# Optimization experiments

Hardware: AMD Instinct MI355X
Metric: run time of the kernel (lower is better)

## Reference

```python
import jax, jax.numpy as jnp
import numpy as np

B = 1_000_000  # batch size
A = 40         # number of CelebA face attributes
GAMMA = 2.0
EPS = 1e-12


def setup_inputs() -> dict:
    key = jax.random.key(0)
    k1, k2, k3 = jax.random.split(key, 3)
    inputs = jax.random.uniform(k1, (B, A), dtype=jnp.float32)  # probabilities
    targets = jax.random.randint(k2, (A, B), 0, 2, dtype=jnp.int32)  # binary labels, attr-first layout
    attr_loss_weight = jax.random.uniform(k3, (A,), dtype=jnp.float32) + 0.5  # positive per-attr weights
    return {"inputs": inputs, "targets": targets, "attr_loss_weight": attr_loss_weight}


def reference(inputs, targets, attr_loss_weight):
    # inputs: [B, A] probabilities; targets: [A, B] binary labels
    t = targets.T.astype(inputs.dtype)                      # [B, A]
    p = jnp.clip(inputs, EPS, 1.0 - EPS)
    bce = -(t * jnp.log(p) + (1.0 - t) * jnp.log1p(-p))     # elementwise BCE
    w = attr_loss_weight[None, :] * jnp.power(1.0 - inputs, GAMMA)  # focal weight
    # per-sample mean over attributes (F.binary_cross_entropy default), summed over batch
    loss = jnp.sum(jnp.mean(w * bce, axis=1))
    return loss
```

## Files before the change

kernel.cpp:

```cpp
#include <hip/hip_runtime.h>

#define NB 1000000
#define NA 40
#define TILE 256
#define NTILES ((NB + TILE - 1) / TILE)
#define NEG_LN2_OVER_A (-0.017328679513998632f)

__global__ __launch_bounds__(256, 4) void focal_loss_kernel(
    const float* __restrict__ inputs,
    const int*   __restrict__ targets,
    const float* __restrict__ attr_w,
    float* __restrict__ out)
{
    __shared__ unsigned int s_t[NA * 65];
    __shared__ float s_aw[NA];
    __shared__ float s_red[TILE / 64];

    const int t  = threadIdx.x;
    const int b0 = blockIdx.x * TILE;

    if (t < NA) s_aw[t] = attr_w[t] * NEG_LN2_OVER_A;

    float acc = 0.0f;

    if (blockIdx.x != NTILES - 1) {
        int4 v[10];
        #pragma unroll
        for (int j = 0; j < 10; ++j) {
            const int q  = t + TILE * j;
            const int a  = q >> 6;
            const int t4 = q & 63;
            v[j] = *(const int4*)(targets + (size_t)a * NB + (b0 + 4 * t4));
        }
        const float4* in4 = (const float4*)inputs + (size_t)b0 * 10;
        float4 xv[10];
        #pragma unroll
        for (int j = 0; j < 10; ++j) xv[j] = in4[t + TILE * j];

        #pragma unroll
        for (int j = 0; j < 10; ++j) {
            const int q  = t + TILE * j;
            const int a  = q >> 6;
            const int t4 = q & 63;
            s_t[a * 65 + t4] =  (unsigned)(v[j].x & 1)        | ((unsigned)(v[j].y & 1) << 8)
                             | ((unsigned)(v[j].z & 1) << 16) | ((unsigned)(v[j].w & 1) << 24);
        }
        __syncthreads();

        const unsigned char* st8 = (const unsigned char*)s_t;
        #pragma unroll
        for (int j = 0; j < 10; ++j) {
            const int f = t + TILE * j;
            const int s = f / 10;
            const int r = 4 * (f - s * 10);
            const float xs[4] = {xv[j].x, xv[j].y, xv[j].z, xv[j].w};
            #pragma unroll
            for (int k = 0; k < 4; ++k) {
                const float x   = xs[k];
                const float om  = 1.0f - x;
                const float w   = s_aw[r + k] * (om * om);
                const float p   = fmaxf(x,  1e-12f);
                const float q0  = fmaxf(om, 1e-12f);
                const float sel = st8[(r + k) * 260 + s] ? p : q0;
                acc = fmaf(w, __log2f(sel), acc);
            }
        }
    } else {
        #pragma unroll
        for (int j = 0; j < 10; ++j) {
            const int q  = t + TILE * j;
            const int a  = q >> 6;
            const int t4 = q & 63;
            const int base = b0 + 4 * t4;
            unsigned int pack = 0;
            for (int k = 0; k < 4; ++k)
                if (base + k < NB)
                    pack |= (unsigned)(targets[(size_t)a * NB + base + k] & 1) << (8 * k);
            s_t[a * 65 + t4] = pack;
        }
        __syncthreads();
        const unsigned char* st8 = (const unsigned char*)s_t;
        const float4* in4 = (const float4*)inputs + (size_t)b0 * 10;
        #pragma unroll
        for (int j = 0; j < 10; ++j) {
            const int f = t + TILE * j;
            const int s = f / 10;
            const int r = 4 * (f - s * 10);
            if (b0 + s < NB) {
                const float4 x4 = in4[f];
                const float xs[4] = {x4.x, x4.y, x4.z, x4.w};
                #pragma unroll
                for (int k = 0; k < 4; ++k) {
                    const float x   = xs[k];
                    const float om  = 1.0f - x;
                    const float w   = s_aw[r + k] * (om * om);
                    const float p   = fmaxf(x,  1e-12f);
                    const float q0  = fmaxf(om, 1e-12f);
                    const float sel = st8[(r + k) * 260 + s] ? p : q0;
                    acc = fmaf(w, __log2f(sel), acc);
                }
            }
        }
    }

    float vsum = acc;
    #pragma unroll
    for (int off = 32; off > 0; off >>= 1)
        vsum += __shfl_xor(vsum, off, 64);
    if ((t & 63) == 0) s_red[t >> 6] = vsum;
    __syncthreads();
    if (t == 0) {
        float r2 = 0.0f;
        #pragma unroll
        for (int w2 = 0; w2 < TILE / 64; ++w2) r2 += s_red[w2];
        atomicAdd(out, r2);
    }
}

extern "C" void kernel_launch(void* const* d_in, const int* in_sizes, int n_in,
                              void* d_out, int out_size, void* d_ws, size_t ws_size,
                              hipStream_t stream) {
    const float* inputs  = (const float*)d_in[0];
    const int*   targets = (const int*)d_in[1];
    const float* attr_w  = (const float*)d_in[2];
    float* out = (float*)d_out;
    hipMemsetAsync(out, 0, sizeof(float), stream);
    focal_loss_kernel<<<dim3(NTILES), dim3(TILE), 0, stream>>>(inputs, targets, attr_w, out);
}
```

Before: 325.2 us.

## Process four tiles per block with double-buffered target prefetch

Each block now handles four consecutive 256-sample tiles, prefetching the next tile's targets into registers during compute and staging the packed bits in a double-buffered LDS array. This aims to hide global load latency and amortize block setup and the final atomic. The grid shrinks roughly fourfold, which reduces the number of resident waves available to hide latency and adds a serial dependency within each block.

```diff
diff --git a/kernel.cpp b/kernel.cpp
--- a/kernel.cpp
+++ b/kernel.cpp
@@ -3,7 +3,9 @@
 #define NB 1000000
 #define NA 40
 #define TILE 256
-#define NTILES ((NB + TILE - 1) / TILE)
+#define G 4
+#define SPB (TILE * G)
+#define NBLK ((NB + SPB - 1) / SPB)
 #define NEG_LN2_OVER_A (-0.017328679513998632f)
 
 __global__ __launch_bounds__(256, 4) void focal_loss_kernel(
@@ -12,83 +14,57 @@
     const float* __restrict__ attr_w,
     float* __restrict__ out)
 {
-    __shared__ unsigned int s_t[NA * 65];
+    __shared__ unsigned int s_t[2][NA * 65];
     __shared__ float s_aw[NA];
     __shared__ float s_red[TILE / 64];
 
     const int t  = threadIdx.x;
-    const int b0 = blockIdx.x * TILE;
+    const int B0 = blockIdx.x * SPB;
 
     if (t < NA) s_aw[t] = attr_w[t] * NEG_LN2_OVER_A;
 
     float acc = 0.0f;
 
-    if (blockIdx.x != NTILES - 1) {
-        int4 v[10];
-        #pragma unroll
-        for (int j = 0; j < 10; ++j) {
-            const int q  = t + TILE * j;
-            const int a  = q >> 6;
-            const int t4 = q & 63;
-            v[j] = *(const int4*)(targets + (size_t)a * NB + (b0 + 4 * t4));
-        }
-        const float4* in4 = (const float4*)inputs + (size_t)b0 * 10;
+    if (blockIdx.x != NBLK - 1) {
+        int4   v[10];
         float4 xv[10];
-        #pragma unroll
-        for (int j = 0; j < 10; ++j) xv[j] = in4[t + TILE * j];
+        const float4* in4 = (const float4*)inputs;
 
         #pragma unroll
         for (int j = 0; j < 10; ++j) {
-            const int q  = t + TILE * j;
-            const int a  = q >> 6;
-            const int t4 = q & 63;
-            s_t[a * 65 + t4] =  (unsigned)(v[j].x & 1)        | ((unsigned)(v[j].y & 1) << 8)
-                             | ((unsigned)(v[j].z & 1) << 16) | ((unsigned)(v[j].w & 1) << 24);
+            const int q = t + TILE * j, a = q >> 6, t4 = q & 63;
+            v[j] = *(const int4*)(targets + (size_t)a * NB + (B0 + 4 * t4));
+        }
+        #pragma unroll
+        for (int j = 0; j < 10; ++j)
+            xv[j] = in4[(size_t)B0 * 10 + t + TILE * j];
+        #pragma unroll
+        for (int j = 0; j < 10; ++j) {
+            const int q = t + TILE * j, a = q >> 6, t4 = q & 63;
+            s_t[0][a * 65 + t4] = (unsigned)(v[j].x & 1)        | ((unsigned)(v[j].y & 1) << 8)
+                                | ((unsigned)(v[j].z & 1) << 16) | ((unsigned)(v[j].w & 1) << 24);
         }
         __syncthreads();
 
-        const unsigned char* st8 = (const unsigned char*)s_t;
         #pragma unroll
-        for (int j = 0; j < 10; ++j) {
-            const int f = t + TILE * j;
-            const int s = f / 10;
-            const int r = 4 * (f - s * 10);
-            const float xs[4] = {xv[j].x, xv[j].y, xv[j].z, xv[j].w};
+        for (int g = 0; g < G; ++g) {
+            const int bt_next = B0 + TILE * (g + 1);
+
+            if (g < G - 1) {
+                #pragma unroll
+                for (int j = 0; j < 10; ++j) {
+                    const int q = t + TILE * j, a = q >> 6, t4 = q & 63;
+                    v[j] = *(const int4*)(targets + (size_t)a * NB + (bt_next + 4 * t4));
+                }
+            }
+
+            const unsigned char* st8 = (const unsigned char*)s_t[g & 1];
             #pragma unroll
-            for (int k = 0; k < 4; ++k) {
-                const float x   = xs[k];
-                const float om  = 1.0f - x;
-                const float w   = s_aw[r + k] * (om * om);
-                const float p   = fmaxf(x,  1e-12f);
-                const float q0  = fmaxf(om, 1e-12f);
-                const float sel = st8[(r + k) * 260 + s] ? p : q0;
-                acc = fmaf(w, __log2f(sel), acc);
-            }
-        }
-    } else {
-        #pragma unroll
-        for (int j = 0; j < 10; ++j) {
-            const int q  = t + TILE * j;
-            const int a  = q >> 6;
-            const int t4 = q & 63;
-            const int base = b0 + 4 * t4;
-            unsigned int pack = 0;
-            for (int k = 0; k < 4; ++k)
-                if (base + k < NB)
-                    pack |= (unsigned)(targets[(size_t)a * NB + base + k] & 1) << (8 * k);
-            s_t[a * 65 + t4] = pack;
-        }
-        __syncthreads();
-        const unsigned char* st8 = (const unsigned char*)s_t;
-        const float4* in4 = (const float4*)inputs + (size_t)b0 * 10;
-        #pragma unroll
-        for (int j = 0; j < 10; ++j) {
-            const int f = t + TILE * j;
-            const int s = f / 10;
-            const int r = 4 * (f - s * 10);
-            if (b0 + s < NB) {
-                const float4 x4 = in4[f];
-                const float xs[4] = {x4.x, x4.y, x4.z, x4.w};
+            for (int j = 0; j < 10; ++j) {
+                const int f = t + TILE * j;
+                const int s = f / 10;
+                const int r = 4 * (f - s * 10);
+                const float xs[4] = {xv[j].x, xv[j].y, xv[j].z, xv[j].w};
                 #pragma unroll
                 for (int k = 0; k < 4; ++k) {
                     const float x   = xs[k];
@@ -98,6 +74,59 @@
                     const float q0  = fmaxf(om, 1e-12f);
                     const float sel = st8[(r + k) * 260 + s] ? p : q0;
                     acc = fmaf(w, __log2f(sel), acc);
+                }
+            }
+
+            if (g < G - 1) {
+                #pragma unroll
+                for (int j = 0; j < 10; ++j)
+                    xv[j] = in4[(size_t)bt_next * 10 + t + TILE * j];
+                #pragma unroll
+                for (int j = 0; j < 10; ++j) {
+                    const int q = t + TILE * j, a = q >> 6, t4 = q & 63;
+                    s_t[(g + 1) & 1][a * 65 + t4] =
+                          (unsigned)(v[j].x & 1)        | ((unsigned)(v[j].y & 1) << 8)
+                        | ((unsigned)(v[j].z & 1) << 16) | ((unsigned)(v[j].w & 1) << 24);
+                }
+                __syncthreads();
+            }
+        }
+    } else {
+        for (int g = 0; g < G; ++g) {
+            const int bt = B0 + TILE * g;
+            if (bt >= NB) break;
+            __syncthreads();
+            #pragma unroll
+            for (int j = 0; j < 10; ++j) {
+                const int q = t + TILE * j, a = q >> 6, t4 = q & 63;
+                const int base = bt + 4 * t4;
+                unsigned int pack = 0;
+                for (int k = 0; k < 4; ++k)
+                    if (base + k < NB)
+                        pack |= (unsigned)(targets[(size_t)a * NB + base + k] & 1) << (8 * k);
+                s_t[0][a * 65 + t4] = pack;
+            }
+            __syncthreads();
+            const unsigned char* st8 = (const unsigned char*)s_t[0];
+            const float4* in4t = (const float4*)inputs + (size_t)bt * 10;
+            #pragma unroll
+            for (int j = 0; j < 10; ++j) {
+                const int f = t + TILE * j;
+                const int s = f / 10;
+                const int r = 4 * (f - s * 10);
+                if (bt + s < NB) {
+                    const float4 x4 = in4t[f];
+                    const float xs[4] = {x4.x, x4.y, x4.z, x4.w};
+                    #pragma unroll
+                    for (int k = 0; k < 4; ++k) {
+                        const float x   = xs[k];
+                        const float om  = 1.0f - x;
+                        const float w   = s_aw[r + k] * (om * om);
+                        const float p   = fmaxf(x,  1e-12f);
+                        const float q0  = fmaxf(om, 1e-12f);
+                        const float sel = st8[(r + k) * 260 + s] ? p : q0;
+                        acc = fmaf(w, __log2f(sel), acc);
+                    }
                 }
             }
         }
@@ -125,5 +154,5 @@
     const float* attr_w  = (const float*)d_in[2];
     float* out = (float*)d_out;
     hipMemsetAsync(out, 0, sizeof(float), stream);
-    focal_loss_kernel<<<dim3(NTILES), dim3(TILE), 0, stream>>>(inputs, targets, attr_w, out);
+    focal_loss_kernel<<<dim3(NBLK), dim3(TILE), 0, stream>>>(inputs, targets, attr_w, out);
 }
```

Result: slower. 350.3 us (+7.7%).

## Persistent blocks with double-buffered async global-to-LDS target loads

Applied to the files above, without the earlier changes.

Replaces the one-tile-per-block grid with 768 persistent 128-thread blocks, each looping over a contiguous range of 128-sample tiles. Target tiles are copied straight into a double-buffered LDS array with global_load_lds, and the next tile is prefetched while the current one is computed. Each thread now owns one sample row (10 float4 loads) and reads its 40 targets directly from LDS, so the byte-packing step goes away. The aim is to hide global-memory latency and cut launch and packing overhead. In exchange, far fewer waves are resident, the per-thread input loads are strided and less coalesced, and correctness depends on the async LDS copies finishing before the barrier.

```diff
diff --git a/kernel.cpp b/kernel.cpp
--- a/kernel.cpp
+++ b/kernel.cpp
@@ -2,103 +2,123 @@
 
 #define NB 1000000
 #define NA 40
-#define TILE 256
-#define NTILES ((NB + TILE - 1) / TILE)
+#define BTH 128
+#define NT_FULL (NB / BTH)
+#define TAIL_START (NT_FULL * BTH)
+#define TAIL_N (NB - TAIL_START)
+#define NBLK 768
+#define QT (NT_FULL / NBLK)
+#define RT (NT_FULL % NBLK)
 #define NEG_LN2_OVER_A (-0.017328679513998632f)
 
-__global__ __launch_bounds__(256, 4) void focal_loss_kernel(
+
+typedef __attribute__((address_space(1))) const void gas_t;
+typedef __attribute__((address_space(3))) void las_t;
+
+__device__ __forceinline__ void gll16(const void* g, void* l) {
+    __builtin_amdgcn_global_load_lds((gas_t*)g, (las_t*)l, 16, 0, 0);
+}
+
+__global__ __launch_bounds__(BTH, 2) void focal_loss_kernel(
     const float* __restrict__ inputs,
     const int*   __restrict__ targets,
     const float* __restrict__ attr_w,
     float* __restrict__ out)
 {
-    __shared__ unsigned int s_t[NA * 65];
+    __shared__ unsigned int s_t[2][NA * BTH];
     __shared__ float s_aw[NA];
-    __shared__ float s_red[TILE / 64];
+    __shared__ float s_red[BTH / 64];
 
-    const int t  = threadIdx.x;
-    const int b0 = blockIdx.x * TILE;
+    const int t = threadIdx.x;
+    const int w = t >> 6;
+    const int l = t & 63;
 
     if (t < NA) s_aw[t] = attr_w[t] * NEG_LN2_OVER_A;
 
+    const int b  = blockIdx.x;
+    const int t0 = b * QT + (b < RT ? b : RT);
+    const int nt = QT + (b < RT ? 1 : 0);
+
     float acc = 0.0f;
+    const float4* in4 = (const float4*)inputs;
 
-    if (blockIdx.x != NTILES - 1) {
-        int4 v[10];
+    float4 xv[10];
+
+    {
+        const int b0 = t0 * BTH;
+        #pragma unroll
+        for (int r = 0; r < 10; ++r) {
+            const int i = w * 10 + r;
+            const int a = 2 * i + (l >> 5);
+            const int s = b0 + 4 * (l & 31);
+            gll16(targets + (size_t)a * NB + s,
+                  (char*)&s_t[0][0] + (size_t)i * 1024);
+        }
+        #pragma unroll
+        for (int j = 0; j < 10; ++j)
+            xv[j] = in4[(size_t)(b0 + t) * 10 + j];
+    }
+    __syncthreads();
+
+    int buf = 0;
+    for (int it = 0; it < nt; ++it) {
+        if (it + 1 < nt) {
+            const int b0n = (t0 + it + 1) * BTH;
+            #pragma unroll
+            for (int r = 0; r < 10; ++r) {
+                const int i = w * 10 + r;
+                const int a = 2 * i + (l >> 5);
+                const int s = b0n + 4 * (l & 31);
+                gll16(targets + (size_t)a * NB + s,
+                      (char*)&s_t[buf ^ 1][0] + (size_t)i * 1024);
+            }
+        }
+
+        const unsigned int* st = &s_t[buf][0];
         #pragma unroll
         for (int j = 0; j < 10; ++j) {
-            const int q  = t + TILE * j;
-            const int a  = q >> 6;
-            const int t4 = q & 63;
-            v[j] = *(const int4*)(targets + (size_t)a * NB + (b0 + 4 * t4));
-        }
-        const float4* in4 = (const float4*)inputs + (size_t)b0 * 10;
-        float4 xv[10];
-        #pragma unroll
-        for (int j = 0; j < 10; ++j) xv[j] = in4[t + TILE * j];
-
-        #pragma unroll
-        for (int j = 0; j < 10; ++j) {
-            const int q  = t + TILE * j;
-            const int a  = q >> 6;
-            const int t4 = q & 63;
-            s_t[a * 65 + t4] =  (unsigned)(v[j].x & 1)        | ((unsigned)(v[j].y & 1) << 8)
-                             | ((unsigned)(v[j].z & 1) << 16) | ((unsigned)(v[j].w & 1) << 24);
-        }
-        __syncthreads();
-
-        const unsigned char* st8 = (const unsigned char*)s_t;
-        #pragma unroll
-        for (int j = 0; j < 10; ++j) {
-            const int f = t + TILE * j;
-            const int s = f / 10;
-            const int r = 4 * (f - s * 10);
             const float xs[4] = {xv[j].x, xv[j].y, xv[j].z, xv[j].w};
             #pragma unroll
             for (int k = 0; k < 4; ++k) {
+                const int a   = 4 * j + k;
                 const float x   = xs[k];
                 const float om  = 1.0f - x;
-                const float w   = s_aw[r + k] * (om * om);
+                const float wgt = s_aw[a] * (om * om);
                 const float p   = fmaxf(x,  1e-12f);
                 const float q0  = fmaxf(om, 1e-12f);
-                const float sel = st8[(r + k) * 260 + s] ? p : q0;
-                acc = fmaf(w, __log2f(sel), acc);
+                const float sel = st[a * BTH + t] ? p : q0;
+                acc = fmaf(wgt, __log2f(sel), acc);
             }
         }
-    } else {
+
+        if (it + 1 < nt) {
+            const int b0n = (t0 + it + 1) * BTH;
+            #pragma unroll
+            for (int j = 0; j < 10; ++j)
+                xv[j] = in4[(size_t)(b0n + t) * 10 + j];
+        }
+        __syncthreads();
+        buf ^= 1;
+    }
+
+    if (b == NBLK - 1 && t < TAIL_N) {
+        const int s = TAIL_START + t;
+        float4 tx[10];
+        #pragma unroll
+        for (int j = 0; j < 10; ++j) tx[j] = in4[(size_t)s * 10 + j];
         #pragma unroll
         for (int j = 0; j < 10; ++j) {
-            const int q  = t + TILE * j;
-            const int a  = q >> 6;
-            const int t4 = q & 63;
-            const int base = b0 + 4 * t4;
-            unsigned int pack = 0;
-            for (int k = 0; k < 4; ++k)
-                if (base + k < NB)
-                    pack |= (unsigned)(targets[(size_t)a * NB + base + k] & 1) << (8 * k);
-            s_t[a * 65 + t4] = pack;
-        }
-        __syncthreads();
-        const unsigned char* st8 = (const unsigned char*)s_t;
-        const float4* in4 = (const float4*)inputs + (size_t)b0 * 10;
-        #pragma unroll
-        for (int j = 0; j < 10; ++j) {
-            const int f = t + TILE * j;
-            const int s = f / 10;
-            const int r = 4 * (f - s * 10);
-            if (b0 + s < NB) {
-                const float4 x4 = in4[f];
-                const float xs[4] = {x4.x, x4.y, x4.z, x4.w};
-                #pragma unroll
-                for (int k = 0; k < 4; ++k) {
-                    const float x   = xs[k];
-                    const float om  = 1.0f - x;
-                    const float w   = s_aw[r + k] * (om * om);
-                    const float p   = fmaxf(x,  1e-12f);
-                    const float q0  = fmaxf(om, 1e-12f);
-                    const float sel = st8[(r + k) * 260 + s] ? p : q0;
-                    acc = fmaf(w, __log2f(sel), acc);
-                }
+            const float xs[4] = {tx[j].x, tx[j].y, tx[j].z, tx[j].w};
+            #pragma unroll
+            for (int k = 0; k < 4; ++k) {
+                const int a   = 4 * j + k;
+                const float x   = xs[k];
+                const float om  = 1.0f - x;
+                const float wgt = s_aw[a] * (om * om);
+                const float p   = fmaxf(x,  1e-12f);
+                const float q0  = fmaxf(om, 1e-12f);
+                const float sel = targets[(size_t)a * NB + s] ? p : q0;
+                acc = fmaf(wgt, __log2f(sel), acc);
             }
         }
     }
@@ -107,14 +127,9 @@
     #pragma unroll
     for (int off = 32; off > 0; off >>= 1)
         vsum += __shfl_xor(vsum, off, 64);
-    if ((t & 63) == 0) s_red[t >> 6] = vsum;
+    if (l == 0) s_red[w] = vsum;
     __syncthreads();
-    if (t == 0) {
-        float r2 = 0.0f;
-        #pragma unroll
-        for (int w2 = 0; w2 < TILE / 64; ++w2) r2 += s_red[w2];
-        atomicAdd(out, r2);
-    }
+    if (t == 0) atomicAdd(out, s_red[0] + s_red[1]);
 }
 
 extern "C" void kernel_launch(void* const* d_in, const int* in_sizes, int n_in,
@@ -125,5 +140,5 @@
     const float* attr_w  = (const float*)d_in[2];
     float* out = (float*)d_out;
     hipMemsetAsync(out, 0, sizeof(float), stream);
-    focal_loss_kernel<<<dim3(NTILES), dim3(TILE), 0, stream>>>(inputs, targets, attr_w, out);
+    focal_loss_kernel<<<dim3(NBLK), dim3(BTH), 0, stream>>>(inputs, targets, attr_w, out);
 }
```

Result: no change. 330.4 us (+1.6%).

## Map one sample per thread and drop shared-memory target transpose

Applied to the files above, without the earlier changes.

Replaces the tiled shared-memory transpose of packed targets with a one-thread-per-sample scheme. Each thread reads its own 40 input probabilities as float4s and reads targets straight from global memory with coalesced column accesses. Loads are software-pipelined three groups ahead of the compute, and occupancy is raised to 8 blocks per CU. This removes the LDS writes, byte reads and barrier, but each thread's input loads are now strided by 160 bytes, so a wave touches many cache lines per load instruction.

```diff
diff --git a/kernel.cpp b/kernel.cpp
--- a/kernel.cpp
+++ b/kernel.cpp
@@ -2,106 +2,59 @@
 
 #define NB 1000000
 #define NA 40
-#define TILE 256
-#define NTILES ((NB + TILE - 1) / TILE)
+#define BTH 256
+#define NBLK ((NB + BTH - 1) / BTH)
 #define NEG_LN2_OVER_A (-0.017328679513998632f)
 
-__global__ __launch_bounds__(256, 4) void focal_loss_kernel(
+__global__ __launch_bounds__(BTH, 8) void focal_loss_kernel(
     const float* __restrict__ inputs,
     const int*   __restrict__ targets,
     const float* __restrict__ attr_w,
     float* __restrict__ out)
 {
-    __shared__ unsigned int s_t[NA * 65];
     __shared__ float s_aw[NA];
-    __shared__ float s_red[TILE / 64];
+    __shared__ float s_red[BTH / 64];
 
-    const int t  = threadIdx.x;
-    const int b0 = blockIdx.x * TILE;
+    const int t = threadIdx.x;
+    if (t < NA) s_aw[t] = attr_w[t] * NEG_LN2_OVER_A;
+    __syncthreads();
 
-    if (t < NA) s_aw[t] = attr_w[t] * NEG_LN2_OVER_A;
+    const int s  = blockIdx.x * BTH + t;
+    const int ok = (s < NB);
+    const int sc = ok ? s : (NB - 1);
 
-    float acc = 0.0f;
+    const float4* xr = (const float4*)(inputs + (size_t)sc * NA);
 
-    if (blockIdx.x != NTILES - 1) {
-        int4 v[10];
-        #pragma unroll
-        for (int j = 0; j < 10; ++j) {
-            const int q  = t + TILE * j;
-            const int a  = q >> 6;
-            const int t4 = q & 63;
-            v[j] = *(const int4*)(targets + (size_t)a * NB + (b0 + 4 * t4));
+    float4 xq[4];
+    int    tq[4][4];
+    float  acc = 0.0f;
+
+    #pragma unroll
+    for (int g = 0; g < 13; ++g) {
+        if (g < 10) {
+            const int sl = g & 3;
+            xq[sl] = xr[g];
+            #pragma unroll
+            for (int k = 0; k < 4; ++k)
+                tq[sl][k] = targets[(size_t)(4 * g + k) * NB + sc];
         }
-        const float4* in4 = (const float4*)inputs + (size_t)b0 * 10;
-        float4 xv[10];
-        #pragma unroll
-        for (int j = 0; j < 10; ++j) xv[j] = in4[t + TILE * j];
-
-        #pragma unroll
-        for (int j = 0; j < 10; ++j) {
-            const int q  = t + TILE * j;
-            const int a  = q >> 6;
-            const int t4 = q & 63;
-            s_t[a * 65 + t4] =  (unsigned)(v[j].x & 1)        | ((unsigned)(v[j].y & 1) << 8)
-                             | ((unsigned)(v[j].z & 1) << 16) | ((unsigned)(v[j].w & 1) << 24);
-        }
-        __syncthreads();
-
-        const unsigned char* st8 = (const unsigned char*)s_t;
-        #pragma unroll
-        for (int j = 0; j < 10; ++j) {
-            const int f = t + TILE * j;
-            const int s = f / 10;
-            const int r = 4 * (f - s * 10);
-            const float xs[4] = {xv[j].x, xv[j].y, xv[j].z, xv[j].w};
+        if (g >= 3) {
+            const int gc = g - 3;
+            const int sl = gc & 3;
+            const float xs[4] = {xq[sl].x, xq[sl].y, xq[sl].z, xq[sl].w};
             #pragma unroll
             for (int k = 0; k < 4; ++k) {
                 const float x   = xs[k];
                 const float om  = 1.0f - x;
-                const float w   = s_aw[r + k] * (om * om);
+                const float wgt = s_aw[4 * gc + k] * (om * om);
                 const float p   = fmaxf(x,  1e-12f);
                 const float q0  = fmaxf(om, 1e-12f);
-                const float sel = st8[(r + k) * 260 + s] ? p : q0;
-                acc = fmaf(w, __log2f(sel), acc);
-            }
-        }
-    } else {
-        #pragma unroll
-        for (int j = 0; j < 10; ++j) {
-            const int q  = t + TILE * j;
-            const int a  = q >> 6;
-            const int t4 = q & 63;
-            const int base = b0 + 4 * t4;
-            unsigned int pack = 0;
-            for (int k = 0; k < 4; ++k)
-                if (base + k < NB)
-                    pack |= (unsigned)(targets[(size_t)a * NB + base + k] & 1) << (8 * k);
-            s_t[a * 65 + t4] = pack;
-        }
-        __syncthreads();
-        const unsigned char* st8 = (const unsigned char*)s_t;
-        const float4* in4 = (const float4*)inputs + (size_t)b0 * 10;
-        #pragma unroll
-        for (int j = 0; j < 10; ++j) {
-            const int f = t + TILE * j;
-            const int s = f / 10;
-            const int r = 4 * (f - s * 10);
-            if (b0 + s < NB) {
-                const float4 x4 = in4[f];
-                const float xs[4] = {x4.x, x4.y, x4.z, x4.w};
-                #pragma unroll
-                for (int k = 0; k < 4; ++k) {
-                    const float x   = xs[k];
-                    const float om  = 1.0f - x;
-                    const float w   = s_aw[r + k] * (om * om);
-                    const float p   = fmaxf(x,  1e-12f);
-                    const float q0  = fmaxf(om, 1e-12f);
-                    const float sel = st8[(r + k) * 260 + s] ? p : q0;
-                    acc = fmaf(w, __log2f(sel), acc);
-                }
+                const float sel = tq[sl][k] ? p : q0;
+                acc = fmaf(wgt, __log2f(sel), acc);
             }
         }
     }
+    if (!ok) acc = 0.0f;
 
     float vsum = acc;
     #pragma unroll
@@ -112,7 +65,7 @@
     if (t == 0) {
         float r2 = 0.0f;
         #pragma unroll
-        for (int w2 = 0; w2 < TILE / 64; ++w2) r2 += s_red[w2];
+        for (int w2 = 0; w2 < BTH / 64; ++w2) r2 += s_red[w2];
         atomicAdd(out, r2);
     }
 }
@@ -125,5 +78,5 @@
     const float* attr_w  = (const float*)d_in[2];
     float* out = (float*)d_out;
     hipMemsetAsync(out, 0, sizeof(float), stream);
-    focal_loss_kernel<<<dim3(NTILES), dim3(TILE), 0, stream>>>(inputs, targets, attr_w, out);
+    focal_loss_kernel<<<dim3(NBLK), dim3(BTH), 0, stream>>>(inputs, targets, attr_w, out);
 }
```

Result: no change. 331.7 us (+2.0%).
